# Kernel tuning notes

Hardware: AMD Instinct MI355X
Metric: run time of the kernel (lower is better)

Reference implementation:

```python
import jax, jax.numpy as jnp
import numpy as np

NH, K = 16, 4  # num_heads, num_points


def _ln(x, g, b):
    m = x.mean(-1, keepdims=True)
    v = jnp.var(x, axis=-1, keepdims=True)
    return (x - m) / jnp.sqrt(v + 1e-5) * g + b


def setup_inputs() -> dict:
    key = jax.random.key(0)
    ks = jax.random.split(key, 12)
    B, S, D = 16, 1024, 1024
    HD = D // NH
    def lin(k, fi, fo, scale=1.0):
        return jax.random.normal(k, (fi, fo), jnp.float32) * (scale / np.sqrt(fi))
    z = lambda n: jnp.zeros((n,), jnp.float32)
    return {
        "source": jax.random.normal(ks[0], (B, S, D), jnp.float32),
        "target": jax.random.normal(ks[1], (B, S, D), jnp.float32),
        "Wq": lin(ks[2], D, D), "bq": z(D),
        "Wo1": lin(ks[3], HD, 64), "bo1": z(64),
        "Wo2": lin(ks[4], 64, 2 * K, 0.1), "bo2": z(2 * K),
        "Wa": lin(ks[5], HD, K), "ba": z(K),
        "Wv": lin(ks[6], D, D), "bv": z(D),
        "Wout": lin(ks[7], D, D), "bout": z(D),
        "gq": jnp.ones((D,), jnp.float32), "bq_ln": z(D),
        "gkv": jnp.ones((D,), jnp.float32), "bkv_ln": z(D),
        "gffn": jnp.ones((D,), jnp.float32), "bffn_ln": z(D),
        "W1": lin(ks[8], D, 4 * D), "b1": z(4 * D),
        "W2": lin(ks[9], 4 * D, D), "b2": z(D),
    }


def _forward(source, target, Wq, bq, Wo1, bo1, Wo2, bo2, Wa, ba, Wv, bv,
             Wout, bout, gq, bq_ln, gkv, bkv_ln, gffn, bffn_ln, W1, b1, W2, b2):
    B, S, D = source.shape
    HD = D // NH
    Hs = int(round(S ** 0.5)); Ws = Hs  # S = H*W square grid

    q_norm = _ln(source, gq, bq_ln)
    v_norm = _ln(target, gkv, bkv_ln)
    q = (q_norm @ Wq + bq).reshape(B, S, NH, HD)
    # value map per head: (B, NH, H, W, HD)
    v = (v_norm @ Wv + bv).reshape(B, Hs, Ws, NH, HD).transpose(0, 3, 1, 2, 4)
    v_flat = v.reshape(B, NH, Hs * Ws, HD)

    # learned offsets: tanh(MLP(q)) * 0.5, in normalized [-1,1] coords
    h = jax.nn.relu(q @ Wo1 + bo1)
    off = jnp.tanh((h @ Wo2 + bo2).reshape(B, S, NH, K, 2)) * 0.5

    # reference grid: ref_grid[i*W+j] = (ref_x[j], ref_y[i])
    rx = jnp.linspace(-1.0, 1.0, Ws)
    ry = jnp.linspace(-1.0, 1.0, Hs)
    gx, gy = jnp.meshgrid(rx, ry)  # 'xy' indexing
    ref = jnp.stack([gx, gy], -1).reshape(S, 2)
    pts = ref[None, :, None, None, :] + off  # (B, S, NH, K, 2), last dim = (x, y)

    # grid_sample, bilinear, align_corners=True, padding_mode='zeros'
    x = (pts[..., 0] + 1.0) * 0.5 * (Ws - 1)
    y = (pts[..., 1] + 1.0) * 0.5 * (Hs - 1)
    x = jnp.moveaxis(x, 1, 2)  # (B, NH, S, K)
    y = jnp.moveaxis(y, 1, 2)
    x0 = jnp.floor(x); y0 = jnp.floor(y)
    wx1 = x - x0; wy1 = y - y0
    x0i = x0.astype(jnp.int32); y0i = y0.astype(jnp.int32)

    def gather(xi, yi, w):
        m = (xi >= 0) & (xi <= Ws - 1) & (yi >= 0) & (yi <= Hs - 1)
        idx = jnp.clip(yi, 0, Hs - 1) * Ws + jnp.clip(xi, 0, Ws - 1)
        g = jnp.take_along_axis(v_flat, idx.reshape(B, NH, S * K, 1), axis=2)
        return g.reshape(B, NH, S, K, HD) * (w * m)[..., None]

    sampled = (gather(x0i, y0i, (1.0 - wx1) * (1.0 - wy1))
               + gather(x0i + 1, y0i, wx1 * (1.0 - wy1))
               + gather(x0i, y0i + 1, (1.0 - wx1) * wy1)
               + gather(x0i + 1, y0i + 1, wx1 * wy1))  # (B, NH, S, K, HD)

    attn = jax.nn.softmax(q @ Wa + ba, axis=-1)  # (B, S, NH, K)
    head_out = jnp.einsum('bsnk,bnskd->bsnd', attn, sampled).reshape(B, S, D)

    src = source + (head_out @ Wout + bout)
    f = jax.nn.gelu(_ln(src, gffn, bffn_ln) @ W1 + b1, approximate=False)
    return src + (f @ W2 + b2)


def reference(source, target, Wq, bq, Wo1, bo1, Wo2, bo2, Wa, ba, Wv, bv,
              Wout, bout, gq, bq_ln, gkv, bkv_ln, gffn, bffn_ln, W1, b1, W2, b2):
    return _forward(source, target, Wq, bq, Wo1, bo1, Wo2, bo2, Wa, ba, Wv, bv,
                    Wout, bout, gq, bq_ln, gkv, bkv_ln, gffn, bffn_ln, W1, b1, W2, b2)
```

## Files before the change

### kernel.cpp

```cpp
#include <hip/hip_runtime.h>

typedef __attribute__((ext_vector_type(8))) short short8;
typedef __attribute__((ext_vector_type(16))) float f32x16;

#define DEV __device__ __forceinline__

DEV float bf2f(unsigned short u) { return __uint_as_float(((unsigned)u) << 16); }
DEV unsigned short f2bf(float f) {
  unsigned u = __float_as_uint(f);
  u += 0x7FFF + ((u >> 16) & 1);
  return (unsigned short)(u >> 16);
}

#define GLOAD_LDS16(gptr, lptr)                                                              \
  __builtin_amdgcn_global_load_lds((const __attribute__((address_space(1))) void*)(gptr),   \
                                   (__attribute__((address_space(3))) void*)(lptr), 16, 0, 0)

__global__ __launch_bounds__(256) void wt_transpose_bf16(const float* __restrict__ W,
                                                         unsigned short* __restrict__ Wt,
                                                         int K, int N) {
  __shared__ float t[32][33];
  int k0 = blockIdx.x * 32, n0 = blockIdx.y * 32;
  int tx = threadIdx.x, ty = threadIdx.y;
#pragma unroll
  for (int i = 0; i < 4; ++i)
    t[ty + 8 * i][tx] = W[(long)(k0 + ty + 8 * i) * N + n0 + tx];
  __syncthreads();
#pragma unroll
  for (int i = 0; i < 4; ++i)
    Wt[(long)(n0 + ty + 8 * i) * K + k0 + tx] = f2bf(t[tx][ty + 8 * i]);
}

__global__ __launch_bounds__(256) void ln_to_bf16(const float* __restrict__ x,
                                                  const float* __restrict__ g,
                                                  const float* __restrict__ b,
                                                  unsigned short* __restrict__ y) {
  const long row = blockIdx.x;
  const int tid = threadIdx.x;
  float4 v = *(const float4*)(x + row * 1024 + tid * 4);
  float s = v.x + v.y + v.z + v.w;
  float s2 = v.x * v.x + v.y * v.y + v.z * v.z + v.w * v.w;
#pragma unroll
  for (int o = 32; o > 0; o >>= 1) { s += __shfl_down(s, o); s2 += __shfl_down(s2, o); }
  __shared__ float red[8];
  __shared__ float mv[2];
  int wv = tid >> 6, ln = tid & 63;
  if (ln == 0) { red[wv] = s; red[4 + wv] = s2; }
  __syncthreads();
  if (tid == 0) {
    float a = red[0] + red[1] + red[2] + red[3];
    float q = red[4] + red[5] + red[6] + red[7];
    float mean = a * (1.f / 1024.f);
    mv[0] = mean;
    mv[1] = rsqrtf(q * (1.f / 1024.f) - mean * mean + 1e-5f);
  }
  __syncthreads();
  float mean = mv[0], rstd = mv[1];
  float4 gg = *(const float4*)(g + tid * 4);
  float4 bb = *(const float4*)(b + tid * 4);
  ushort4 o;
  o.x = f2bf((v.x - mean) * rstd * gg.x + bb.x);
  o.y = f2bf((v.y - mean) * rstd * gg.y + bb.y);
  o.z = f2bf((v.z - mean) * rstd * gg.z + bb.z);
  o.w = f2bf((v.w - mean) * rstd * gg.w + bb.w);
  *(ushort4*)(y + row * 1024 + tid * 4) = o;
}

template <int EPI>
__global__ __launch_bounds__(512, 4) void gemm_bf16(const unsigned short* __restrict__ A,
                                                    const unsigned short* __restrict__ Bt,
                                                    const float* __restrict__ bias,
                                                    const float* __restrict__ res,
                                                    void* __restrict__ out,
                                                    int N, int K, int ldb) {
  __shared__ __align__(16) char smem[49152];
  const int tid = threadIdx.x;
  const int wave = tid >> 6, lane = tid & 63;
  const int wm = wave >> 1, wn = wave & 1;
  const long col0 = (long)blockIdx.x * 128;
  const long row0 = (long)blockIdx.y * 256;

  f32x16 acc[2][2];
#pragma unroll
  for (int i = 0; i < 2; ++i)
#pragma unroll
    for (int n = 0; n < 2; ++n)
#pragma unroll
      for (int r = 0; r < 16; ++r) acc[i][n][r] = 0.f;

  const int rin = lane >> 3, ch = lane & 7;
  const int kg = ch ^ rin;

  for (int kt = 0; kt < K; kt += 64) {
#pragma unroll
    for (int i = 0; i < 4; ++i) {
      const int c = wave * 4 + i;
      const int r = c * 8 + rin;
      GLOAD_LDS16(A + (row0 + r) * (long)K + kt + kg * 8, smem + c * 1024);
    }
#pragma unroll
    for (int i = 0; i < 2; ++i) {
      const int c = wave * 2 + i;
      const int r = c * 8 + rin;
      GLOAD_LDS16(Bt + (col0 + r) * (long)ldb + kt + kg * 8, smem + 32768 + c * 1024);
    }
    asm volatile("s_waitcnt vmcnt(0)" ::: "memory");
    __syncthreads();
#pragma unroll
    for (int ks = 0; ks < 4; ++ks) {
      short8 af[2], bfr[2];
      const int kc = ks * 2 + (lane >> 5);
#pragma unroll
      for (int mi = 0; mi < 2; ++mi) {
        const int rowa = wm * 64 + mi * 32 + (lane & 31);
        af[mi] = *(const short8*)(smem + rowa * 128 + (kc ^ (rowa & 7)) * 16);
      }
#pragma unroll
      for (int ni = 0; ni < 2; ++ni) {
        const int rowb = wn * 64 + ni * 32 + (lane & 31);
        bfr[ni] = *(const short8*)(smem + 32768 + rowb * 128 + (kc ^ (rowb & 7)) * 16);
      }
#pragma unroll
      for (int mi = 0; mi < 2; ++mi)
#pragma unroll
        for (int ni = 0; ni < 2; ++ni)
          acc[mi][ni] =
              __builtin_amdgcn_mfma_f32_32x32x16_bf16(af[mi], bfr[ni], acc[mi][ni], 0, 0, 0);
    }
    __syncthreads();
  }

  const int lc = lane & 31, lh = lane >> 5;
#pragma unroll
  for (int mi = 0; mi < 2; ++mi) {
#pragma unroll
    for (int ni = 0; ni < 2; ++ni) {
      const long gcol = col0 + wn * 64 + ni * 32 + lc;
      const float bvv = (EPI == 5) ? 0.f : bias[gcol];
#pragma unroll
      for (int reg = 0; reg < 16; ++reg) {
        const long grow = row0 + wm * 64 + mi * 32 + (reg & 3) + 8 * (reg >> 2) + 4 * lh;
        float val = acc[mi][ni][reg] + bvv;
        if (EPI == 0) {
          ((float*)out)[grow * N + gcol] = val;
        } else if (EPI == 1) {
          const int b_ = (int)(grow >> 10), hw = (int)(grow & 1023);
          const int nh = (int)(gcol >> 6), hd = (int)(gcol & 63);
          ((unsigned short*)out)[((long)(b_ * 16 + nh) << 16) + hw * 64 + hd] = f2bf(val);
        } else if (EPI == 2) {
          ((float*)out)[grow * N + gcol] = val + res[grow * N + gcol];
        } else if (EPI == 3) {
          float gl = 0.5f * val * (1.f + erff(val * 0.70710678118654752f));
          ((unsigned short*)out)[grow * N + gcol] = f2bf(gl);
        } else {
          ((float*)out)[grow * N + gcol] = val + res[grow * N + gcol];
        }
      }
    }
  }
}

__global__ __launch_bounds__(256) void offset_attn_mlp(
    const float* __restrict__ qf,
    const float* __restrict__ Wo1, const float* __restrict__ bo1,
    const float* __restrict__ Wo2, const float* __restrict__ bo2,
    const float* __restrict__ Wa, const float* __restrict__ ba,
    float* __restrict__ coords) {
  const int r = blockIdx.x * 256 + threadIdx.x;
  const int s = (r >> 4) & 1023;

  float qr[64];
  const float* qp = qf + (long)r * 64;
#pragma unroll
  for (int i = 0; i < 16; ++i) *(float4*)(qr + 4 * i) = *(const float4*)(qp + 4 * i);

  float off[8];
#pragma unroll
  for (int o = 0; o < 8; ++o) off[o] = bo2[o];

#pragma unroll 1
  for (int jj = 0; jj < 8; ++jj) {
    float hacc[8];
#pragma unroll
    for (int o = 0; o < 8; ++o) hacc[o] = bo1[jj * 8 + o];
#pragma unroll
    for (int i = 0; i < 64; ++i) {
      const float qv = qr[i];
#pragma unroll
      for (int o = 0; o < 8; ++o) hacc[o] = fmaf(qv, Wo1[i * 64 + jj * 8 + o], hacc[o]);
    }
#pragma unroll
    for (int jo = 0; jo < 8; ++jo) {
      const float hj = fmaxf(hacc[jo], 0.f);
      const int j = jj * 8 + jo;
#pragma unroll
      for (int o = 0; o < 8; ++o) off[o] = fmaf(hj, Wo2[j * 8 + o], off[o]);
    }
  }

  float lg[4];
#pragma unroll
  for (int k = 0; k < 4; ++k) lg[k] = ba[k];
#pragma unroll
  for (int i = 0; i < 64; ++i) {
    const float qv = qr[i];
#pragma unroll
    for (int k = 0; k < 4; ++k) lg[k] = fmaf(qv, Wa[i * 4 + k], lg[k]);
  }
  const float mx = fmaxf(fmaxf(lg[0], lg[1]), fmaxf(lg[2], lg[3]));
  const float e0 = expf(lg[0] - mx), e1 = expf(lg[1] - mx), e2 = expf(lg[2] - mx),
              e3 = expf(lg[3] - mx);
  const float inv = 1.f / (e0 + e1 + e2 + e3);

  const float sx = (float)(s & 31), sy = (float)(s >> 5);
  float4 xv, yv, av;
  xv.x = sx + tanhf(off[0]) * 7.75f; yv.x = sy + tanhf(off[1]) * 7.75f;
  xv.y = sx + tanhf(off[2]) * 7.75f; yv.y = sy + tanhf(off[3]) * 7.75f;
  xv.z = sx + tanhf(off[4]) * 7.75f; yv.z = sy + tanhf(off[5]) * 7.75f;
  xv.w = sx + tanhf(off[6]) * 7.75f; yv.w = sy + tanhf(off[7]) * 7.75f;
  av.x = e0 * inv; av.y = e1 * inv; av.z = e2 * inv; av.w = e3 * inv;
  float* cp = coords + (long)r * 16;
  *(float4*)(cp + 0) = xv;
  *(float4*)(cp + 4) = yv;
  *(float4*)(cp + 8) = av;
}

__global__ __launch_bounds__(256) void deform_gather(
    const unsigned short* __restrict__ v_flat, const float* __restrict__ coords,
    unsigned short* __restrict__ head_out) {
  const int tid = threadIdx.x, wave = tid >> 6, lane = tid & 63;
  const int m = blockIdx.x * 4 + wave;
  const int b = m >> 14, nh = (m >> 10) & 15, s = m & 1023;
  const long r = (long)(b * 1024 + s) * 16 + nh;

  float cf = 0.f;
  if (lane < 12) cf = coords[r * 16 + lane];
  const unsigned short* vb = v_flat + ((long)(b * 16 + nh) << 16);

  float o = 0.f;
#pragma unroll
  for (int k = 0; k < 4; ++k) {
    const float xp = __shfl(cf, k), yp = __shfl(cf, 4 + k), ak = __shfl(cf, 8 + k);
    const float x0f = floorf(xp), y0f = floorf(yp);
    const int x0 = (int)x0f, y0 = (int)y0f;
    const float wx1 = xp - x0f, wy1 = yp - y0f;
    const float wx0 = 1.f - wx1, wy0 = 1.f - wy1;
    float smp = 0.f;
#pragma unroll
    for (int cn = 0; cn < 4; ++cn) {
      const int xi = x0 + (cn & 1), yi = y0 + (cn >> 1);
      const float w = (cn & 1 ? wx1 : wx0) * (cn >> 1 ? wy1 : wy0);
      const bool msk = (xi >= 0) & (xi <= 31) & (yi >= 0) & (yi <= 31);
      const int xc = min(max(xi, 0), 31), yc = min(max(yi, 0), 31);
      const float vv = bf2f(vb[(yc * 32 + xc) * 64 + lane]);
      smp = fmaf(vv, msk ? w : 0.f, smp);
    }
    o = fmaf(ak, smp, o);
  }
  head_out[r * 64 + lane] = f2bf(o);
}

extern "C" void kernel_launch(void* const* d_in, const int* in_sizes, int n_in,
                              void* d_out, int out_size, void* d_ws, size_t ws_size,
                              hipStream_t stream) {
  const float* source = (const float*)d_in[0];
  const float* target = (const float*)d_in[1];
  const float* Wq = (const float*)d_in[2];
  const float* bq = (const float*)d_in[3];
  const float* Wo1 = (const float*)d_in[4];
  const float* bo1 = (const float*)d_in[5];
  const float* Wo2 = (const float*)d_in[6];
  const float* bo2 = (const float*)d_in[7];
  const float* Wa = (const float*)d_in[8];
  const float* ba = (const float*)d_in[9];
  const float* Wv = (const float*)d_in[10];
  const float* bv = (const float*)d_in[11];
  const float* Wout = (const float*)d_in[12];
  const float* bout = (const float*)d_in[13];
  const float* gq = (const float*)d_in[14];
  const float* bq_ln = (const float*)d_in[15];
  const float* gkv = (const float*)d_in[16];
  const float* bkv_ln = (const float*)d_in[17];
  const float* gffn = (const float*)d_in[18];
  const float* bffn_ln = (const float*)d_in[19];
  const float* W1 = (const float*)d_in[20];
  const float* b1 = (const float*)d_in[21];
  const float* W2 = (const float*)d_in[22];
  const float* b2 = (const float*)d_in[23];

  char* ws = (char*)d_ws;
  const size_t MB = 1u << 20;
  if (ws_size < 150 * MB) return;

  unsigned short* q_norm = (unsigned short*)(ws + 0);
  unsigned short* v_flat = (unsigned short*)(ws + 0);
  unsigned short* v_norm = (unsigned short*)(ws + 32 * MB);
  float* coords = (float*)(ws + 32 * MB);
  unsigned short* ffn_in = (unsigned short*)(ws + 32 * MB);
  float* qf = (float*)(ws + 64 * MB);
  unsigned short* head_out = (unsigned short*)(ws + 64 * MB);
  unsigned short* f_buf = (unsigned short*)(ws + 64 * MB);
  unsigned short* Wq_t = (unsigned short*)(ws + 128 * MB);
  unsigned short* Wv_t = (unsigned short*)(ws + 130 * MB);
  unsigned short* Wout_t = (unsigned short*)(ws + 132 * MB);
  unsigned short* W1_t = (unsigned short*)(ws + 134 * MB);
  unsigned short* W2_t = (unsigned short*)(ws + 142 * MB);
  float* src = (float*)d_out;

  dim3 tb(32, 8);
  wt_transpose_bf16<<<dim3(32, 32), tb, 0, stream>>>(Wq, Wq_t, 1024, 1024);
  wt_transpose_bf16<<<dim3(32, 32), tb, 0, stream>>>(Wv, Wv_t, 1024, 1024);
  wt_transpose_bf16<<<dim3(32, 32), tb, 0, stream>>>(Wout, Wout_t, 1024, 1024);
  wt_transpose_bf16<<<dim3(32, 128), tb, 0, stream>>>(W1, W1_t, 1024, 4096);
  wt_transpose_bf16<<<dim3(128, 32), tb, 0, stream>>>(W2, W2_t, 4096, 1024);

  ln_to_bf16<<<16384, 256, 0, stream>>>(source, gq, bq_ln, q_norm);
  ln_to_bf16<<<16384, 256, 0, stream>>>(target, gkv, bkv_ln, v_norm);

  gemm_bf16<0><<<dim3(8, 64), 512, 0, stream>>>(q_norm, Wq_t, bq, nullptr, qf, 1024, 1024, 1024);
  gemm_bf16<1><<<dim3(8, 64), 512, 0, stream>>>(v_norm, Wv_t, bv, nullptr, v_flat, 1024, 1024, 1024);

  offset_attn_mlp<<<1024, 256, 0, stream>>>(qf, Wo1, bo1, Wo2, bo2, Wa, ba, coords);
  deform_gather<<<65536, 256, 0, stream>>>(v_flat, coords, head_out);

  gemm_bf16<2><<<dim3(8, 64), 512, 0, stream>>>(head_out, Wout_t, bout, source, src, 1024, 1024, 1024);

  ln_to_bf16<<<16384, 256, 0, stream>>>(src, gffn, bffn_ln, ffn_in);

  gemm_bf16<3><<<dim3(16, 64), 512, 0, stream>>>(ffn_in, W1_t, b1, nullptr, f_buf, 2048, 1024, 1024);
  gemm_bf16<2><<<dim3(8, 64), 512, 0, stream>>>(f_buf, W2_t, b2, src, src, 1024, 2048, 4096);
  gemm_bf16<3><<<dim3(16, 64), 512, 0, stream>>>(ffn_in, W1_t + (long)2048 * 1024, b1 + 2048,
                                                 nullptr, f_buf, 2048, 1024, 1024);
  gemm_bf16<5><<<dim3(8, 64), 512, 0, stream>>>(f_buf, W2_t + 2048, nullptr, src, src, 1024, 2048, 4096);
}
```

Measured before the change: 766.6 us.

## Switch GEMMs to 128x128 tiles with new LDS swizzle, unsplit FFN when workspace allows

Replaces the 256x128-tile, 512-thread GEMM with a 128x128-tile, 256-thread kernel that uses 32KB of LDS. The grid is reordered so the row tile varies fastest, and the LDS XOR swizzle now uses (row>>1)&7 to change the bank-conflict pattern. When the workspace holds at least 182MB, the FFN runs as one full-width W1 GEMM and one K=4096 W2 GEMM instead of two halves, which avoids re-reading src and extra launches. Smaller tiles lower per-block data reuse but add blocks and occupancy.

```diff
diff --git a/kernel.cpp b/kernel.cpp
--- a/kernel.cpp
+++ b/kernel.cpp
@@ -67,18 +67,36 @@
 }
 
 template <int EPI>
-__global__ __launch_bounds__(512, 4) void gemm_bf16(const unsigned short* __restrict__ A,
-                                                    const unsigned short* __restrict__ Bt,
-                                                    const float* __restrict__ bias,
-                                                    const float* __restrict__ res,
-                                                    void* __restrict__ out,
-                                                    int N, int K, int ldb) {
-  __shared__ __align__(16) char smem[49152];
+DEV void epi_store(void* out, const float* res, long grow, long gcol, int N, float val) {
+  if (EPI == 0) {
+    ((float*)out)[grow * N + gcol] = val;
+  } else if (EPI == 1) {
+    const int b_ = (int)(grow >> 10), hw = (int)(grow & 1023);
+    const int nh = (int)(gcol >> 6), hd = (int)(gcol & 63);
+    ((unsigned short*)out)[((long)(b_ * 16 + nh) << 16) + hw * 64 + hd] = f2bf(val);
+  } else if (EPI == 2) {
+    ((float*)out)[grow * N + gcol] = val + res[grow * N + gcol];
+  } else if (EPI == 3) {
+    float gl = 0.5f * val * (1.f + erff(val * 0.70710678118654752f));
+    ((unsigned short*)out)[grow * N + gcol] = f2bf(gl);
+  } else {
+    ((float*)out)[grow * N + gcol] = val + res[grow * N + gcol];
+  }
+}
+
+template <int EPI>
+__global__ __launch_bounds__(256, 4) void gemm32(const unsigned short* __restrict__ A,
+                                                 const unsigned short* __restrict__ Bt,
+                                                 const float* __restrict__ bias,
+                                                 const float* __restrict__ res,
+                                                 void* __restrict__ out,
+                                                 int N, int K, int ldb) {
+  __shared__ __align__(16) char smem[32768];
   const int tid = threadIdx.x;
   const int wave = tid >> 6, lane = tid & 63;
   const int wm = wave >> 1, wn = wave & 1;
-  const long col0 = (long)blockIdx.x * 128;
-  const long row0 = (long)blockIdx.y * 256;
+  const long row0 = (long)blockIdx.x * 128;
+  const long col0 = (long)blockIdx.y * 128;
 
   f32x16 acc[2][2];
 #pragma unroll
@@ -89,20 +107,15 @@
       for (int r = 0; r < 16; ++r) acc[i][n][r] = 0.f;
 
   const int rin = lane >> 3, ch = lane & 7;
-  const int kg = ch ^ rin;
 
   for (int kt = 0; kt < K; kt += 64) {
 #pragma unroll
     for (int i = 0; i < 4; ++i) {
       const int c = wave * 4 + i;
       const int r = c * 8 + rin;
+      const int kg = ch ^ ((r >> 1) & 7);
       GLOAD_LDS16(A + (row0 + r) * (long)K + kt + kg * 8, smem + c * 1024);
-    }
-#pragma unroll
-    for (int i = 0; i < 2; ++i) {
-      const int c = wave * 2 + i;
-      const int r = c * 8 + rin;
-      GLOAD_LDS16(Bt + (col0 + r) * (long)ldb + kt + kg * 8, smem + 32768 + c * 1024);
+      GLOAD_LDS16(Bt + (col0 + r) * (long)ldb + kt + kg * 8, smem + 16384 + c * 1024);
     }
     asm volatile("s_waitcnt vmcnt(0)" ::: "memory");
     __syncthreads();
@@ -113,12 +126,12 @@
 #pragma unroll
       for (int mi = 0; mi < 2; ++mi) {
         const int rowa = wm * 64 + mi * 32 + (lane & 31);
-        af[mi] = *(const short8*)(smem + rowa * 128 + (kc ^ (rowa & 7)) * 16);
+        af[mi] = *(const short8*)(smem + rowa * 128 + (kc ^ ((rowa >> 1) & 7)) * 16);
       }
 #pragma unroll
       for (int ni = 0; ni < 2; ++ni) {
         const int rowb = wn * 64 + ni * 32 + (lane & 31);
-        bfr[ni] = *(const short8*)(smem + 32768 + rowb * 128 + (kc ^ (rowb & 7)) * 16);
+        bfr[ni] = *(const short8*)(smem + 16384 + rowb * 128 + (kc ^ ((rowb >> 1) & 7)) * 16);
       }
 #pragma unroll
       for (int mi = 0; mi < 2; ++mi)
@@ -132,7 +145,7 @@
 
   const int lc = lane & 31, lh = lane >> 5;
 #pragma unroll
-  for (int mi = 0; mi < 2; ++mi) {
+  for (int mi = 0; mi < 2; ++mi)
 #pragma unroll
     for (int ni = 0; ni < 2; ++ni) {
       const long gcol = col0 + wn * 64 + ni * 32 + lc;
@@ -140,24 +153,9 @@
 #pragma unroll
       for (int reg = 0; reg < 16; ++reg) {
         const long grow = row0 + wm * 64 + mi * 32 + (reg & 3) + 8 * (reg >> 2) + 4 * lh;
-        float val = acc[mi][ni][reg] + bvv;
-        if (EPI == 0) {
-          ((float*)out)[grow * N + gcol] = val;
-        } else if (EPI == 1) {
-          const int b_ = (int)(grow >> 10), hw = (int)(grow & 1023);
-          const int nh = (int)(gcol >> 6), hd = (int)(gcol & 63);
-          ((unsigned short*)out)[((long)(b_ * 16 + nh) << 16) + hw * 64 + hd] = f2bf(val);
-        } else if (EPI == 2) {
-          ((float*)out)[grow * N + gcol] = val + res[grow * N + gcol];
-        } else if (EPI == 3) {
-          float gl = 0.5f * val * (1.f + erff(val * 0.70710678118654752f));
-          ((unsigned short*)out)[grow * N + gcol] = f2bf(gl);
-        } else {
-          ((float*)out)[grow * N + gcol] = val + res[grow * N + gcol];
-        }
+        epi_store<EPI>(out, res, grow, gcol, N, acc[mi][ni][reg] + bvv);
       }
     }
-  }
 }
 
 __global__ __launch_bounds__(256) void offset_attn_mlp(
@@ -291,20 +289,22 @@
   char* ws = (char*)d_ws;
   const size_t MB = 1u << 20;
   if (ws_size < 150 * MB) return;
+  const bool big = (ws_size >= 182 * MB);
 
   unsigned short* q_norm = (unsigned short*)(ws + 0);
   unsigned short* v_flat = (unsigned short*)(ws + 0);
   unsigned short* v_norm = (unsigned short*)(ws + 32 * MB);
   float* coords = (float*)(ws + 32 * MB);
-  unsigned short* ffn_in = (unsigned short*)(ws + 32 * MB);
   float* qf = (float*)(ws + 64 * MB);
   unsigned short* head_out = (unsigned short*)(ws + 64 * MB);
-  unsigned short* f_buf = (unsigned short*)(ws + 64 * MB);
-  unsigned short* Wq_t = (unsigned short*)(ws + 128 * MB);
-  unsigned short* Wv_t = (unsigned short*)(ws + 130 * MB);
-  unsigned short* Wout_t = (unsigned short*)(ws + 132 * MB);
-  unsigned short* W1_t = (unsigned short*)(ws + 134 * MB);
-  unsigned short* W2_t = (unsigned short*)(ws + 142 * MB);
+  unsigned short* ffn_in = (unsigned short*)(big ? ws + 128 * MB : ws + 32 * MB);
+  unsigned short* f_buf = (unsigned short*)(big ? ws + 0 : ws + 64 * MB);
+  char* wbase = big ? ws + 160 * MB : ws + 128 * MB;
+  unsigned short* Wq_t = (unsigned short*)(wbase + 0);
+  unsigned short* Wv_t = (unsigned short*)(wbase + 2 * MB);
+  unsigned short* Wout_t = (unsigned short*)(wbase + 4 * MB);
+  unsigned short* W1_t = (unsigned short*)(wbase + 6 * MB);
+  unsigned short* W2_t = (unsigned short*)(wbase + 14 * MB);
   float* src = (float*)d_out;
 
   dim3 tb(32, 8);
@@ -317,19 +317,24 @@
   ln_to_bf16<<<16384, 256, 0, stream>>>(source, gq, bq_ln, q_norm);
   ln_to_bf16<<<16384, 256, 0, stream>>>(target, gkv, bkv_ln, v_norm);
 
-  gemm_bf16<0><<<dim3(8, 64), 512, 0, stream>>>(q_norm, Wq_t, bq, nullptr, qf, 1024, 1024, 1024);
-  gemm_bf16<1><<<dim3(8, 64), 512, 0, stream>>>(v_norm, Wv_t, bv, nullptr, v_flat, 1024, 1024, 1024);
+  gemm32<0><<<dim3(128, 8), 256, 0, stream>>>(q_norm, Wq_t, bq, nullptr, qf, 1024, 1024, 1024);
+  gemm32<1><<<dim3(128, 8), 256, 0, stream>>>(v_norm, Wv_t, bv, nullptr, v_flat, 1024, 1024, 1024);
 
   offset_attn_mlp<<<1024, 256, 0, stream>>>(qf, Wo1, bo1, Wo2, bo2, Wa, ba, coords);
   deform_gather<<<65536, 256, 0, stream>>>(v_flat, coords, head_out);
 
-  gemm_bf16<2><<<dim3(8, 64), 512, 0, stream>>>(head_out, Wout_t, bout, source, src, 1024, 1024, 1024);
+  gemm32<2><<<dim3(128, 8), 256, 0, stream>>>(head_out, Wout_t, bout, source, src, 1024, 1024, 1024);
 
   ln_to_bf16<<<16384, 256, 0, stream>>>(src, gffn, bffn_ln, ffn_in);
 
-  gemm_bf16<3><<<dim3(16, 64), 512, 0, stream>>>(ffn_in, W1_t, b1, nullptr, f_buf, 2048, 1024, 1024);
-  gemm_bf16<2><<<dim3(8, 64), 512, 0, stream>>>(f_buf, W2_t, b2, src, src, 1024, 2048, 4096);
-  gemm_bf16<3><<<dim3(16, 64), 512, 0, stream>>>(ffn_in, W1_t + (long)2048 * 1024, b1 + 2048,
+  if (big) {
+    gemm32<3><<<dim3(128, 32), 256, 0, stream>>>(ffn_in, W1_t, b1, nullptr, f_buf, 4096, 1024, 1024);
+    gemm32<2><<<dim3(128, 8), 256, 0, stream>>>(f_buf, W2_t, b2, src, src, 1024, 4096, 4096);
+  } else {
+    gemm32<3><<<dim3(128, 16), 256, 0, stream>>>(ffn_in, W1_t, b1, nullptr, f_buf, 2048, 1024, 1024);
+    gemm32<2><<<dim3(128, 8), 256, 0, stream>>>(f_buf, W2_t, b2, src, src, 1024, 2048, 4096);
+    gemm32<3><<<dim3(128, 16), 256, 0, stream>>>(ffn_in, W1_t + (long)2048 * 1024, b1 + 2048,
                                                  nullptr, f_buf, 2048, 1024, 1024);
-  gemm_bf16<5><<<dim3(8, 64), 512, 0, stream>>>(f_buf, W2_t + 2048, nullptr, src, src, 1024, 2048, 4096);
-}
+    gemm32<5><<<dim3(128, 8), 256, 0, stream>>>(f_buf, W2_t + 2048, nullptr, src, src, 1024, 2048, 4096);
+  }
+}
```

Result: faster. 736.3 us (median of 2 runs) (-3.9%).
